# Kernel tuning notes

Measured on AMD Instinct MI355X. Metric: run time of the kernel, lower is better.

## Reference

```python
import jax, jax.numpy as jnp
import numpy as np

N, D, M = 4096, 2048, 1000
NL = 2048
MAX_ITER = 5


def setup_inputs() -> dict:
    key = jax.random.key(0)
    k1, k2, k3 = jax.random.split(key, 3)
    fc7 = jax.random.normal(k1, (N, D), dtype=jnp.float32)
    # prior probs: softmax over random logits (row-stochastic, like CNN softmax output)
    probs = jax.nn.softmax(jax.random.normal(k2, (N, M), dtype=jnp.float32), axis=-1)
    labs = jax.random.randint(k3, (NL,), 0, M)
    L = jnp.arange(NL)
    U = jnp.arange(NL, N)
    return {"fc7": fc7, "probs": probs, "labs": labs, "L": L, "U": U}


def _get_W_correlation(fc7):
    # Pearson correlation between rows, negatives clipped to zero (set_negative='hard')
    x = fc7 - fc7.mean(axis=1, keepdims=True)
    norms = jnp.linalg.norm(x, axis=1)  # [n]
    W = (x @ x.T) / jnp.outer(norms, norms)  # [n, n]
    return jax.nn.relu(W)


def _init_probs_prior(probs, labs, L, U):
    n, m = probs.shape
    ps = jnp.zeros((n, m), dtype=probs.dtype)
    ps = ps.at[U].set(probs[U])       # unlabeled: CNN prior
    ps = ps.at[L, labs].set(1.0)      # labeled: one-hot
    return ps


def _replicator(W, ps, max_iter):
    def step(p, _):
        q = p * (W @ p)                              # [n, m]
        q = q / jnp.sum(q, axis=1, keepdims=True)
        return q, None
    ps, _ = jax.lax.scan(step, ps, None, length=max_iter)
    return ps


def reference(fc7, probs, labs, L, U):
    W = _get_W_correlation(fc7)
    ps = _init_probs_prior(probs, labs, L, U)
    ps = _replicator(W, ps, MAX_ITER)
    return ps, W
```

## Files before the change

kernel.cpp:

```cpp
#include <hip/hip_runtime.h>
#include <stdint.h>

#define NS 4096
#define DD 2048
#define MC 1000
#define MP 1024
#define NLAB 2048
#define NU 2048

typedef __attribute__((ext_vector_type(8))) short bf16x8;
typedef __attribute__((ext_vector_type(4))) float f32x4;

__device__ inline unsigned short f2bf(float f) {
  union { float f; uint32_t u; } v; v.f = f;
  uint32_t u = v.u;
  u = u + 0x7fffu + ((u >> 16) & 1u);
  return (unsigned short)(u >> 16);
}
__device__ inline float bf2f(unsigned short h) {
  union { uint32_t u; float f; } v; v.u = ((uint32_t)h) << 16;
  return v.f;
}

__device__ inline void gload_lds16(const void* g, void* l) {
  __builtin_amdgcn_global_load_lds(
      (const __attribute__((address_space(1))) void*)g,
      (__attribute__((address_space(3))) void*)l, 16, 0, 0);
}

__device__ inline float block_sum(float v, float* sm, int tid) {
  #pragma unroll
  for (int o = 32; o > 0; o >>= 1) v += __shfl_down(v, o, 64);
  __syncthreads();
  if ((tid & 63) == 0) sm[tid >> 6] = v;
  __syncthreads();
  return sm[0] + sm[1] + sm[2] + sm[3];
}

__global__ void center_norm_k(const float* __restrict__ fc7,
                              unsigned short* __restrict__ Xc,
                              float* __restrict__ invn) {
  __shared__ float sm[4];
  const int row = blockIdx.x;
  const int tid = threadIdx.x;
  const float4* src = (const float4*)(fc7 + (size_t)row * DD);
  float4 a = src[tid * 2];
  float4 b = src[tid * 2 + 1];
  float s = a.x + a.y + a.z + a.w + b.x + b.y + b.z + b.w;
  s = block_sum(s, sm, tid);
  const float mean = s * (1.f / (float)DD);
  float v0 = a.x - mean, v1 = a.y - mean, v2 = a.z - mean, v3 = a.w - mean;
  float v4 = b.x - mean, v5 = b.y - mean, v6 = b.z - mean, v7 = b.w - mean;
  float ss = v0*v0 + v1*v1 + v2*v2 + v3*v3 + v4*v4 + v5*v5 + v6*v6 + v7*v7;
  ss = block_sum(ss, sm, tid);
  if (tid == 0) invn[row] = rsqrtf(ss);
  ushort4 o0 = make_ushort4(f2bf(v0), f2bf(v1), f2bf(v2), f2bf(v3));
  ushort4 o1 = make_ushort4(f2bf(v4), f2bf(v5), f2bf(v6), f2bf(v7));
  ushort4* dst = (ushort4*)(Xc + (size_t)row * DD);
  dst[tid * 2] = o0;
  dst[tid * 2 + 1] = o1;
}

__global__ void gemm_w_sym(const unsigned short* __restrict__ A,
                           const float* __restrict__ invn,
                           float* __restrict__ outF,
                           unsigned short* __restrict__ outBF) {
  __shared__ __align__(16) unsigned short As[64 * 64];
  __shared__ __align__(16) unsigned short Bs[128 * 64];
  const int tid = threadIdx.x;
  const int wv = tid >> 6;
  const int ln = tid & 63;
  const int wr = wv >> 1, wc = wv & 1;

  int b = (blockIdx.x & 7) * 132 + (blockIdx.x >> 3);
  int r = 0;
  while (b >= 32 - (r >> 1)) { b -= 32 - (r >> 1); ++r; }
  const int c = (r >> 1) + b;
  const int rowBase = r * 64;
  const int colBase = c * 128;
  const bool mirror = (c > (r >> 1));
  const int fr = ln & 15, kg = ln >> 4;

  f32x4 acc[2][4];
  f32x4 zz = {0.f, 0.f, 0.f, 0.f};
  #pragma unroll
  for (int i = 0; i < 2; ++i)
    #pragma unroll
    for (int j = 0; j < 4; ++j) acc[i][j] = zz;

  const int lrow = ln >> 3;
  const int lcol = ((ln & 7) ^ lrow) * 8;
  const unsigned short* Ap = A + (size_t)(rowBase + lrow) * DD + lcol;
  const unsigned short* Bp = A + (size_t)(colBase + lrow) * DD + lcol;

  for (int k0 = 0; k0 < DD; k0 += 64) {
    if (k0) __syncthreads();
    #pragma unroll
    for (int u = 0; u < 2; ++u) {
      const int rr = wv * 16 + u * 8;
      gload_lds16(Ap + (size_t)rr * DD + k0, &As[rr * 64]);
    }
    #pragma unroll
    for (int u = 0; u < 4; ++u) {
      const int rr = wv * 32 + u * 8;
      gload_lds16(Bp + (size_t)rr * DD + k0, &Bs[rr * 64]);
    }
    __syncthreads();
    #pragma unroll
    for (int kk = 0; kk < 2; ++kk) {
      bf16x8 af[2], bfr[4];
      #pragma unroll
      for (int i = 0; i < 2; ++i) {
        const int rr = wr * 32 + i * 16 + fr;
        af[i] = *(const bf16x8*)&As[rr * 64 + ((kk * 4 + kg) ^ (rr & 7)) * 8];
      }
      #pragma unroll
      for (int j = 0; j < 4; ++j) {
        const int rr = wc * 64 + j * 16 + fr;
        bfr[j] = *(const bf16x8*)&Bs[rr * 64 + ((kk * 4 + kg) ^ (rr & 7)) * 8];
      }
      #pragma unroll
      for (int i = 0; i < 2; ++i)
        #pragma unroll
        for (int j = 0; j < 4; ++j)
          acc[i][j] = __builtin_amdgcn_mfma_f32_16x16x32_bf16(af[i], bfr[j], acc[i][j], 0, 0, 0);
    }
  }

  const int cr = (ln >> 4) * 4;
  const int cc = ln & 15;
  #pragma unroll
  for (int i = 0; i < 2; ++i) {
    const int rb = rowBase + wr * 32 + i * 16 + cr;
    #pragma unroll
    for (int j = 0; j < 4; ++j) {
      const int cb = colBase + wc * 64 + j * 16 + cc;
      const float ic = invn[cb];
      float v[4];
      #pragma unroll
      for (int u = 0; u < 4; ++u) {
        float x = acc[i][j][u] * invn[rb + u] * ic;
        v[u] = x > 0.f ? x : 0.f;
        const size_t o = (size_t)(rb + u) * NS + cb;
        outF[o] = v[u];
        outBF[o] = f2bf(v[u]);
      }
      if (mirror) {
        const size_t o = (size_t)cb * NS + rb;
        *(float4*)&outF[o] = make_float4(v[0], v[1], v[2], v[3]);
        *(ushort4*)&outBF[o] = make_ushort4(f2bf(v[0]), f2bf(v[1]), f2bf(v[2]), f2bf(v[3]));
      }
    }
  }
}

__global__ void gemm_rep(const unsigned short* __restrict__ pT,
                         const unsigned short* __restrict__ Wbf,
                         float* __restrict__ q0, float* __restrict__ q1,
                         float* __restrict__ q2, float* __restrict__ q3) {
  __shared__ __align__(16) unsigned short As[64 * 64];
  __shared__ __align__(16) unsigned short Bs[128 * 64];
  const int tid = threadIdx.x;
  const int wv = tid >> 6;
  const int ln = tid & 63;
  const int wr = wv >> 1, wc = wv & 1;
  const int rowBase = blockIdx.y * 64;
  const int colBase = blockIdx.x * 128;
  const int kOff = blockIdx.z * 1024;
  float* __restrict__ outF = (blockIdx.z == 0) ? q0 : (blockIdx.z == 1) ? q1
                           : (blockIdx.z == 2) ? q2 : q3;
  const int fr = ln & 15, kg = ln >> 4;

  f32x4 acc[2][4];
  f32x4 zz = {0.f, 0.f, 0.f, 0.f};
  #pragma unroll
  for (int i = 0; i < 2; ++i)
    #pragma unroll
    for (int j = 0; j < 4; ++j) acc[i][j] = zz;

  const int lrow = ln >> 3;
  const int lcol = ((ln & 7) ^ lrow) * 8;
  const unsigned short* Ap = pT + (size_t)(rowBase + lrow) * NS + kOff + lcol;
  const unsigned short* Bp = Wbf + (size_t)(NLAB + colBase + lrow) * NS + kOff + lcol;

  for (int k0 = 0; k0 < 1024; k0 += 64) {
    if (k0) __syncthreads();
    #pragma unroll
    for (int u = 0; u < 2; ++u) {
      const int rr = wv * 16 + u * 8;
      gload_lds16(Ap + (size_t)rr * NS + k0, &As[rr * 64]);
    }
    #pragma unroll
    for (int u = 0; u < 4; ++u) {
      const int rr = wv * 32 + u * 8;
      gload_lds16(Bp + (size_t)rr * NS + k0, &Bs[rr * 64]);
    }
    __syncthreads();
    #pragma unroll
    for (int kk = 0; kk < 2; ++kk) {
      bf16x8 af[2], bfr[4];
      #pragma unroll
      for (int i = 0; i < 2; ++i) {
        const int rr = wr * 32 + i * 16 + fr;
        af[i] = *(const bf16x8*)&As[rr * 64 + ((kk * 4 + kg) ^ (rr & 7)) * 8];
      }
      #pragma unroll
      for (int j = 0; j < 4; ++j) {
        const int rr = wc * 64 + j * 16 + fr;
        bfr[j] = *(const bf16x8*)&Bs[rr * 64 + ((kk * 4 + kg) ^ (rr & 7)) * 8];
      }
      #pragma unroll
      for (int i = 0; i < 2; ++i)
        #pragma unroll
        for (int j = 0; j < 4; ++j)
          acc[i][j] = __builtin_amdgcn_mfma_f32_16x16x32_bf16(af[i], bfr[j], acc[i][j], 0, 0, 0);
    }
  }

  const int cr = (ln >> 4) * 4;
  const int cc = ln & 15;
  #pragma unroll
  for (int i = 0; i < 2; ++i) {
    const int rb = rowBase + wr * 32 + i * 16 + cr;
    #pragma unroll
    for (int j = 0; j < 4; ++j) {
      const int cb = colBase + wc * 64 + j * 16 + cc;
      #pragma unroll
      for (int u = 0; u < 4; ++u)
        outF[(size_t)(rb + u) * NU + cb] = acc[i][j][u];
    }
  }
}

__global__ void init_pT_k(const float* __restrict__ probs, const int* __restrict__ labs,
                          unsigned short* __restrict__ pT) {
  __shared__ float t[32][33];
  const int tx = threadIdx.x, ty = threadIdx.y;
  const int i0 = blockIdx.x * 32, m0 = blockIdx.y * 32;
  const int i = i0 + ty;
  const int m = m0 + tx;
  float v = 0.f;
  if (i < NLAB) v = (m == labs[i]) ? 1.f : 0.f;
  else if (m < MC) v = probs[(size_t)i * MC + m];
  t[ty][tx] = v;
  __syncthreads();
  pT[(size_t)(m0 + ty) * NS + i0 + tx] = f2bf(t[tx][ty]);
}

__global__ void onehot_k(const int* __restrict__ labs, float* __restrict__ ps) {
  const int i = blockIdx.x;
  const int m4 = threadIdx.x * 4;
  if (m4 >= MC) return;
  const int lab = labs[i];
  float4 v;
  v.x = (lab == m4)     ? 1.f : 0.f;
  v.y = (lab == m4 + 1) ? 1.f : 0.f;
  v.z = (lab == m4 + 2) ? 1.f : 0.f;
  v.w = (lab == m4 + 3) ? 1.f : 0.f;
  *(float4*)&ps[(size_t)i * MC + m4] = v;
}

__global__ void colsum_part_k(const float* __restrict__ q0, const float* __restrict__ q1,
                              const float* __restrict__ q2, const float* __restrict__ q3,
                              const unsigned short* __restrict__ pT,
                              float* __restrict__ part) {
  const int i = blockIdx.x * 256 + threadIdx.x;
  const int c = blockIdx.y;
  float s = 0.f;
  #pragma unroll 4
  for (int mm = 0; mm < 64; ++mm) {
    const int m = c * 64 + mm;
    const size_t o = (size_t)m * NU + i;
    const float q = q0[o] + q1[o] + q2[o] + q3[o];
    s += bf2f(pT[(size_t)m * NS + NLAB + i]) * q;
  }
  part[c * NU + i] = s;
}

__global__ void colsum_fin_k(const float* __restrict__ part, float* __restrict__ rsum) {
  const int i = blockIdx.x * 256 + threadIdx.x;
  float s = 0.f;
  #pragma unroll
  for (int c = 0; c < 16; ++c) s += part[c * NU + i];
  rsum[i] = 1.0f / s;
}

__global__ void scale_k(const float* __restrict__ q0, const float* __restrict__ q1,
                        const float* __restrict__ q2, const float* __restrict__ q3,
                        const float* __restrict__ rsum,
                        unsigned short* __restrict__ pT) {
  const int g = blockIdx.x * 256 + threadIdx.x;
  const int idx = g * 4;
  const int i = idx & (NU - 1);
  const int m = idx >> 11;
  float4 a = *(const float4*)(q0 + idx);
  float4 b = *(const float4*)(q1 + idx);
  float4 cc = *(const float4*)(q2 + idx);
  float4 d = *(const float4*)(q3 + idx);
  float4 r = *(const float4*)(rsum + i);
  ushort4 p = *(const ushort4*)(pT + (size_t)m * NS + NLAB + i);
  ushort4 o = make_ushort4(f2bf(bf2f(p.x) * (a.x + b.x + cc.x + d.x) * r.x),
                           f2bf(bf2f(p.y) * (a.y + b.y + cc.y + d.y) * r.y),
                           f2bf(bf2f(p.z) * (a.z + b.z + cc.z + d.z) * r.z),
                           f2bf(bf2f(p.w) * (a.w + b.w + cc.w + d.w) * r.w));
  *(ushort4*)(pT + (size_t)m * NS + NLAB + i) = o;
}

__global__ void final_k(const float* __restrict__ q0, const float* __restrict__ q1,
                        const float* __restrict__ q2, const float* __restrict__ q3,
                        const unsigned short* __restrict__ pT,
                        const float* __restrict__ rsum,
                        float* __restrict__ ps) {
  __shared__ float t[32][33];
  const int tx = threadIdx.x, ty = threadIdx.y;
  const int i0 = blockIdx.x * 32, m0 = blockIdx.y * 32;
  {
    const int m = m0 + ty, i = i0 + tx;
    const size_t o = (size_t)m * NU + i;
    const float q = q0[o] + q1[o] + q2[o] + q3[o];
    t[ty][tx] = bf2f(pT[(size_t)m * NS + NLAB + i]) * q;
  }
  __syncthreads();
  const int i = i0 + ty, m = m0 + tx;
  if (m < MC)
    ps[(size_t)(NLAB + i) * MC + m] = t[tx][ty] * rsum[i];
}

extern "C" void kernel_launch(void* const* d_in, const int* in_sizes, int n_in,
                              void* d_out, int out_size, void* d_ws, size_t ws_size,
                              hipStream_t stream) {
  const float* fc7   = (const float*)d_in[0];
  const float* probs = (const float*)d_in[1];
  const int*   labs  = (const int*)d_in[2];

  char* ws = (char*)d_ws;
  unsigned short* Xc   = (unsigned short*)(ws);
  unsigned short* Wbf  = (unsigned short*)(ws + (16ull << 20));
  unsigned short* pT   = (unsigned short*)(ws + (48ull << 20));
  float*          q0   = (float*)(ws + (56ull << 20));
  float*          q1   = (float*)(ws + (64ull << 20));
  float*          q2   = (float*)(ws + (72ull << 20));
  float*          q3   = (float*)(ws + (80ull << 20));
  float*          invn = (float*)(ws + (88ull << 20));
  float*          rsum = (float*)(ws + (88ull << 20) + (16ull << 10));
  float*          part = (float*)(ws + (88ull << 20) + (32ull << 10));

  float* out_ps = (float*)d_out;
  float* out_W  = out_ps + (size_t)NS * MC;

  center_norm_k<<<NS, 256, 0, stream>>>(fc7, Xc, invn);

  gemm_w_sym<<<1056, 256, 0, stream>>>(Xc, invn, out_W, Wbf);

  init_pT_k<<<dim3(NS / 32, MP / 32), dim3(32, 32), 0, stream>>>(probs, labs, pT);
  onehot_k<<<NLAB, 256, 0, stream>>>(labs, out_ps);

  for (int it = 0; it < 5; ++it) {
    gemm_rep<<<dim3(NU / 128, MP / 64, 4), 256, 0, stream>>>(pT, Wbf, q0, q1, q2, q3);
    colsum_part_k<<<dim3(NU / 256, 16), 256, 0, stream>>>(q0, q1, q2, q3, pT, part);
    colsum_fin_k<<<NU / 256, 256, 0, stream>>>(part, rsum);
    if (it < 4)
      scale_k<<<(MP * NU / 4) / 256, 256, 0, stream>>>(q0, q1, q2, q3, rsum, pT);
    else
      final_k<<<dim3(NU / 32, MP / 32), dim3(32, 32), 0, stream>>>(q0, q1, q2, q3, pT, rsum, out_ps);
  }
}
```

Baseline: 304.7 us.

## Hoist constant labeled-row contribution out of replicator iterations

Labeled rows of the probability matrix stay fixed one-hot vectors, so their contribution W[U,L]·p[L] is computed once before the loop and stored in WL. Each iteration's GEMM then only reduces over the unlabeled half of K. colsum also materializes the product p*q into a buffer so scale and final kernels read one array instead of four partials plus pT. This adds extra fp32 traffic for WL and pq in exchange for halving per-iteration GEMM work.

```diff
diff --git a/kernel.cpp b/kernel.cpp
--- a/kernel.cpp
+++ b/kernel.cpp
@@ -157,7 +157,8 @@
 __global__ void gemm_rep(const unsigned short* __restrict__ pT,
                          const unsigned short* __restrict__ Wbf,
                          float* __restrict__ q0, float* __restrict__ q1,
-                         float* __restrict__ q2, float* __restrict__ q3) {
+                         float* __restrict__ q2, float* __restrict__ q3,
+                         int kBase) {
   __shared__ __align__(16) unsigned short As[64 * 64];
   __shared__ __align__(16) unsigned short Bs[128 * 64];
   const int tid = threadIdx.x;
@@ -166,7 +167,7 @@
   const int wr = wv >> 1, wc = wv & 1;
   const int rowBase = blockIdx.y * 64;
   const int colBase = blockIdx.x * 128;
-  const int kOff = blockIdx.z * 1024;
+  const int kOff = kBase + blockIdx.z * 512;
   float* __restrict__ outF = (blockIdx.z == 0) ? q0 : (blockIdx.z == 1) ? q1
                            : (blockIdx.z == 2) ? q2 : q3;
   const int fr = ln & 15, kg = ln >> 4;
@@ -183,7 +184,7 @@
   const unsigned short* Ap = pT + (size_t)(rowBase + lrow) * NS + kOff + lcol;
   const unsigned short* Bp = Wbf + (size_t)(NLAB + colBase + lrow) * NS + kOff + lcol;
 
-  for (int k0 = 0; k0 < 1024; k0 += 64) {
+  for (int k0 = 0; k0 < 512; k0 += 64) {
     if (k0) __syncthreads();
     #pragma unroll
     for (int u = 0; u < 2; ++u) {
@@ -230,6 +231,18 @@
         outF[(size_t)(rb + u) * NU + cb] = acc[i][j][u];
     }
   }
+}
+
+__global__ void merge_k(const float* __restrict__ q0, const float* __restrict__ q1,
+                        const float* __restrict__ q2, const float* __restrict__ q3,
+                        float* __restrict__ WL) {
+  const int idx = (blockIdx.x * 256 + threadIdx.x) * 4;
+  float4 a = *(const float4*)(q0 + idx);
+  float4 b = *(const float4*)(q1 + idx);
+  float4 c = *(const float4*)(q2 + idx);
+  float4 d = *(const float4*)(q3 + idx);
+  *(float4*)(WL + idx) = make_float4(a.x + b.x + c.x + d.x, a.y + b.y + c.y + d.y,
+                                     a.z + b.z + c.z + d.z, a.w + b.w + c.w + d.w);
 }
 
 __global__ void init_pT_k(const float* __restrict__ probs, const int* __restrict__ labs,
@@ -262,7 +275,9 @@
 
 __global__ void colsum_part_k(const float* __restrict__ q0, const float* __restrict__ q1,
                               const float* __restrict__ q2, const float* __restrict__ q3,
+                              const float* __restrict__ WL,
                               const unsigned short* __restrict__ pT,
+                              float* __restrict__ pq,
                               float* __restrict__ part) {
   const int i = blockIdx.x * 256 + threadIdx.x;
   const int c = blockIdx.y;
@@ -271,8 +286,10 @@
   for (int mm = 0; mm < 64; ++mm) {
     const int m = c * 64 + mm;
     const size_t o = (size_t)m * NU + i;
-    const float q = q0[o] + q1[o] + q2[o] + q3[o];
-    s += bf2f(pT[(size_t)m * NS + NLAB + i]) * q;
+    const float q = q0[o] + q1[o] + q2[o] + q3[o] + WL[o];
+    const float f = bf2f(pT[(size_t)m * NS + NLAB + i]) * q;
+    s += f;
+    pq[o] = f;
   }
   part[c * NU + i] = s;
 }
@@ -285,41 +302,27 @@
   rsum[i] = 1.0f / s;
 }
 
-__global__ void scale_k(const float* __restrict__ q0, const float* __restrict__ q1,
-                        const float* __restrict__ q2, const float* __restrict__ q3,
+__global__ void scale_k(const float* __restrict__ pq,
                         const float* __restrict__ rsum,
                         unsigned short* __restrict__ pT) {
   const int g = blockIdx.x * 256 + threadIdx.x;
   const int idx = g * 4;
   const int i = idx & (NU - 1);
   const int m = idx >> 11;
-  float4 a = *(const float4*)(q0 + idx);
-  float4 b = *(const float4*)(q1 + idx);
-  float4 cc = *(const float4*)(q2 + idx);
-  float4 d = *(const float4*)(q3 + idx);
+  float4 p = *(const float4*)(pq + idx);
   float4 r = *(const float4*)(rsum + i);
-  ushort4 p = *(const ushort4*)(pT + (size_t)m * NS + NLAB + i);
-  ushort4 o = make_ushort4(f2bf(bf2f(p.x) * (a.x + b.x + cc.x + d.x) * r.x),
-                           f2bf(bf2f(p.y) * (a.y + b.y + cc.y + d.y) * r.y),
-                           f2bf(bf2f(p.z) * (a.z + b.z + cc.z + d.z) * r.z),
-                           f2bf(bf2f(p.w) * (a.w + b.w + cc.w + d.w) * r.w));
+  ushort4 o = make_ushort4(f2bf(p.x * r.x), f2bf(p.y * r.y),
+                           f2bf(p.z * r.z), f2bf(p.w * r.w));
   *(ushort4*)(pT + (size_t)m * NS + NLAB + i) = o;
 }
 
-__global__ void final_k(const float* __restrict__ q0, const float* __restrict__ q1,
-                        const float* __restrict__ q2, const float* __restrict__ q3,
-                        const unsigned short* __restrict__ pT,
+__global__ void final_k(const float* __restrict__ pq,
                         const float* __restrict__ rsum,
                         float* __restrict__ ps) {
   __shared__ float t[32][33];
   const int tx = threadIdx.x, ty = threadIdx.y;
   const int i0 = blockIdx.x * 32, m0 = blockIdx.y * 32;
-  {
-    const int m = m0 + ty, i = i0 + tx;
-    const size_t o = (size_t)m * NU + i;
-    const float q = q0[o] + q1[o] + q2[o] + q3[o];
-    t[ty][tx] = bf2f(pT[(size_t)m * NS + NLAB + i]) * q;
-  }
+  t[ty][tx] = pq[(size_t)(m0 + ty) * NU + i0 + tx];
   __syncthreads();
   const int i = i0 + ty, m = m0 + tx;
   if (m < MC)
@@ -341,9 +344,11 @@
   float*          q1   = (float*)(ws + (64ull << 20));
   float*          q2   = (float*)(ws + (72ull << 20));
   float*          q3   = (float*)(ws + (80ull << 20));
-  float*          invn = (float*)(ws + (88ull << 20));
-  float*          rsum = (float*)(ws + (88ull << 20) + (16ull << 10));
-  float*          part = (float*)(ws + (88ull << 20) + (32ull << 10));
+  float*          WL   = (float*)(ws + (88ull << 20));
+  float*          pq   = (float*)(ws + (96ull << 20));
+  float*          invn = (float*)(ws + (104ull << 20));
+  float*          rsum = (float*)(ws + (104ull << 20) + (16ull << 10));
+  float*          part = (float*)(ws + (104ull << 20) + (32ull << 10));
 
   float* out_ps = (float*)d_out;
   float* out_W  = out_ps + (size_t)NS * MC;
@@ -355,13 +360,16 @@
   init_pT_k<<<dim3(NS / 32, MP / 32), dim3(32, 32), 0, stream>>>(probs, labs, pT);
   onehot_k<<<NLAB, 256, 0, stream>>>(labs, out_ps);
 
+  gemm_rep<<<dim3(NU / 128, MP / 64, 4), 256, 0, stream>>>(pT, Wbf, q0, q1, q2, q3, 0);
+  merge_k<<<(MP * NU / 4) / 256, 256, 0, stream>>>(q0, q1, q2, q3, WL);
+
   for (int it = 0; it < 5; ++it) {
-    gemm_rep<<<dim3(NU / 128, MP / 64, 4), 256, 0, stream>>>(pT, Wbf, q0, q1, q2, q3);
-    colsum_part_k<<<dim3(NU / 256, 16), 256, 0, stream>>>(q0, q1, q2, q3, pT, part);
+    gemm_rep<<<dim3(NU / 128, MP / 64, 4), 256, 0, stream>>>(pT, Wbf, q0, q1, q2, q3, NLAB);
+    colsum_part_k<<<dim3(NU / 256, 16), 256, 0, stream>>>(q0, q1, q2, q3, WL, pT, pq, part);
     colsum_fin_k<<<NU / 256, 256, 0, stream>>>(part, rsum);
     if (it < 4)
-      scale_k<<<(MP * NU / 4) / 256, 256, 0, stream>>>(q0, q1, q2, q3, rsum, pT);
+      scale_k<<<(MP * NU / 4) / 256, 256, 0, stream>>>(pq, rsum, pT);
     else
-      final_k<<<dim3(NU / 32, MP / 32), dim3(32, 32), 0, stream>>>(q0, q1, q2, q3, pT, rsum, out_ps);
-  }
-}
+      final_k<<<dim3(NU / 32, MP / 32), dim3(32, 32), 0, stream>>>(pq, rsum, out_ps);
+  }
+}
```

Result: faster. 282.3 us (-7.3%).
